# Kernel tuning notes

Hardware: AMD Instinct MI355X
Metric: run time of the kernel (lower is better)

The kernel has to match this reference:

```python
import jax, jax.numpy as jnp
import numpy as np

H = 16          # num_heads
W = 256         # sliding window size
LN_EPS = 1e-6
ROPE_BASE = 10000.0


def layer_norm(x, g, b):
    m = jnp.mean(x, axis=-1, keepdims=True)
    v = jnp.mean((x - m) ** 2, axis=-1, keepdims=True)
    return (x - m) * jax.lax.rsqrt(v + LN_EPS) * g + b


def rope(x):
    # x: [B, S, H, hd]; rotate-half RoPE
    S, hd = x.shape[1], x.shape[-1]
    inv_freq = 1.0 / (ROPE_BASE ** (jnp.arange(0, hd, 2, dtype=jnp.float32) / hd))
    ang = jnp.arange(S, dtype=jnp.float32)[:, None] * inv_freq[None, :]  # [S, hd/2]
    cos = jnp.concatenate([jnp.cos(ang), jnp.cos(ang)], axis=-1)[None, :, None, :]
    sin = jnp.concatenate([jnp.sin(ang), jnp.sin(ang)], axis=-1)[None, :, None, :]
    x1, x2 = jnp.split(x, 2, axis=-1)
    rot = jnp.concatenate([-x2, x1], axis=-1)
    return x * cos + rot * sin


def setup_inputs() -> dict:
    key = jax.random.key(0)
    ks = jax.random.split(key, 12)
    B, S, D, I = 2, 2048, 1024, 4096
    s = 0.02
    return {
        "hidden_states": jax.random.normal(ks[0], (B, S, D), jnp.float32),
        "wq": jax.random.normal(ks[1], (D, D), jnp.float32) * s,
        "wk": jax.random.normal(ks[2], (D, D), jnp.float32) * s,
        "wv": jax.random.normal(ks[3], (D, D), jnp.float32) * s,
        "wo": jax.random.normal(ks[4], (D, D), jnp.float32) * s,
        "w1": jax.random.normal(ks[5], (D, I), jnp.float32) * s,
        "w2": jax.random.normal(ks[6], (I, D), jnp.float32) * s,
        "w3": jax.random.normal(ks[7], (D, I), jnp.float32) * s,
        "ln1_g": jnp.ones((D,), jnp.float32),
        "ln1_b": jnp.zeros((D,), jnp.float32),
        "ln2_g": jnp.ones((D,), jnp.float32),
        "ln2_b": jnp.zeros((D,), jnp.float32),
    }


def reference(hidden_states, wq, wk, wv, wo, w1, w2, w3, ln1_g, ln1_b, ln2_g, ln2_b):
    B, S, D = hidden_states.shape
    hd = D // H

    # --- attention sub-block ---
    residual = hidden_states
    x = layer_norm(hidden_states, ln1_g, ln1_b)
    q = (x @ wq).reshape(B, S, H, hd)
    k = (x @ wk).reshape(B, S, H, hd)
    v = (x @ wv).reshape(B, S, H, hd)
    q, k = rope(q), rope(k)

    scores = jnp.einsum("bqhd,bkhd->bhqk", q, k) / jnp.sqrt(jnp.float32(hd))
    idx = jnp.arange(S)
    rel = idx[:, None] - idx[None, :]          # i - j
    mask = (rel >= 0) & (rel < W)              # causal sliding window
    scores = jnp.where(mask[None, None], scores, jnp.float32(-1e9))
    attn = jax.nn.softmax(scores, axis=-1)
    ctx = jnp.einsum("bhqk,bkhd->bqhd", attn, v).reshape(B, S, D)
    hidden_states = residual + ctx @ wo

    # --- SwiGLU MLP sub-block ---
    residual = hidden_states
    x = layer_norm(hidden_states, ln2_g, ln2_b)
    mlp = (jax.nn.silu(x @ w1) * (x @ w3)) @ w2
    return residual + mlp
```

## Files before the change

### kernel.cpp

```cpp
#include <hip/hip_runtime.h>
#include <hip/hip_bf16.h>

typedef __bf16 bf16_t;
typedef __bf16 bf16x4 __attribute__((ext_vector_type(4)));
typedef __bf16 bf16x8 __attribute__((ext_vector_type(8)));
typedef float f32x4 __attribute__((ext_vector_type(4)));

#define LN_EPS 1e-6f

__device__ __forceinline__ void gl2lds16(const void* g, void* l) {
    __builtin_amdgcn_global_load_lds(
        (const __attribute__((address_space(1))) void*)g,
        (__attribute__((address_space(3))) void*)l, 16, 0, 0);
}

__global__ void transpose_cvt_kernel(const float* __restrict__ in, bf16_t* __restrict__ out,
                                     int R, int C) {
    __shared__ float tile[32][33];
    int tx = threadIdx.x & 31;
    int ty = threadIdx.x >> 5;
    int r0 = blockIdx.y * 32;
    int c0 = blockIdx.x * 32;
#pragma unroll
    for (int i = 0; i < 4; i++) {
        int r = ty + i * 8;
        tile[r][tx] = in[(size_t)(r0 + r) * C + (c0 + tx)];
    }
    __syncthreads();
#pragma unroll
    for (int i = 0; i < 4; i++) {
        int r = ty + i * 8;
        out[(size_t)(c0 + r) * R + (r0 + tx)] = (bf16_t)tile[tx][r];
    }
}

__global__ void ln_kernel(const float* __restrict__ x, const float* __restrict__ g,
                          const float* __restrict__ bb, bf16_t* __restrict__ out, int D) {
    int row = blockIdx.x;
    int t = threadIdx.x;
    const float4* xr = reinterpret_cast<const float4*>(x + (size_t)row * D);
    float4 v = xr[t];
    float s = v.x + v.y + v.z + v.w;
    __shared__ float sbuf[4];
    __shared__ float sbuf2[4];
    int wave = t >> 6, lane = t & 63;
#pragma unroll
    for (int o = 32; o > 0; o >>= 1) s += __shfl_xor(s, o);
    if (lane == 0) sbuf[wave] = s;
    __syncthreads();
    float mean = (sbuf[0] + sbuf[1] + sbuf[2] + sbuf[3]) / (float)D;
    float d0 = v.x - mean, d1 = v.y - mean, d2 = v.z - mean, d3 = v.w - mean;
    float sq = d0 * d0 + d1 * d1 + d2 * d2 + d3 * d3;
#pragma unroll
    for (int o = 32; o > 0; o >>= 1) sq += __shfl_xor(sq, o);
    if (lane == 0) sbuf2[wave] = sq;
    __syncthreads();
    float var = (sbuf2[0] + sbuf2[1] + sbuf2[2] + sbuf2[3]) / (float)D;
    float inv = rsqrtf(var + LN_EPS);
    float4 gv = reinterpret_cast<const float4*>(g)[t];
    float4 bv = reinterpret_cast<const float4*>(bb)[t];
    bf16_t* o0 = out + (size_t)row * D + t * 4;
    o0[0] = (bf16_t)(d0 * inv * gv.x + bv.x);
    o0[1] = (bf16_t)(d1 * inv * gv.y + bv.y);
    o0[2] = (bf16_t)(d2 * inv * gv.z + bv.z);
    o0[3] = (bf16_t)(d3 * inv * gv.w + bv.w);
}

#define G4_BK 64

template <int EPI>
__launch_bounds__(256, 2) __global__
void gemm4_kernel(const bf16_t* __restrict__ A, const bf16_t* __restrict__ Bt,
                  float* __restrict__ Cf, const float* __restrict__ aux,
                  const bf16_t* __restrict__ auxb, bf16_t* __restrict__ Cb,
                  int M, int N, int K, int lda, int ldb) {
    __shared__ __align__(16) bf16_t As[128 * G4_BK];
    __shared__ __align__(16) bf16_t Bs[128 * G4_BK];
    const int t = threadIdx.x;
    const int wave = t >> 6, lane = t & 63;
    const int lr = lane & 15, quad = lane >> 4;
    const int wm = (wave >> 1) * 64, wn = (wave & 1) * 64;

    const int gx = gridDim.x, gy = gridDim.y;
    const int nwg = gx * gy;
    const int lin = blockIdx.y * gx + blockIdx.x;
    const int qch = nwg >> 3;
    const int sw = (lin & 7) * qch + (lin >> 3);
    const int m0 = (sw / gy) * 128;
    const int n0 = (sw % gy) * 128;
    const int koff = blockIdx.z * K;

    const int srow = t >> 3;
    const int sslot = (t & 7) ^ (srow & 7);
    const bf16_t* agp = A + (size_t)(m0 + srow) * lda + koff + sslot * 8;
    const bf16_t* bgp = Bt + (size_t)(n0 + srow) * ldb + koff + sslot * 8;
    bf16_t* asl = As + t * 8;
    bf16_t* bsl = Bs + t * 8;

    int aoff[4][2], boff[4][2];
#pragma unroll
    for (int f = 0; f < 4; f++)
#pragma unroll
        for (int s = 0; s < 2; s++) {
            int ra = wm + f * 16 + lr;
            int rb = wn + f * 16 + lr;
            aoff[f][s] = ra * G4_BK + (((s * 4 + quad) ^ (ra & 7)) << 3);
            boff[f][s] = rb * G4_BK + (((s * 4 + quad) ^ (rb & 7)) << 3);
        }

    f32x4 acc[4][4];
#pragma unroll
    for (int mi = 0; mi < 4; mi++)
#pragma unroll
        for (int ni = 0; ni < 4; ni++) acc[mi][ni] = 0.f;

    for (int k0 = 0; k0 < K; k0 += G4_BK) {
#pragma unroll
        for (int i = 0; i < 4; i++)
            gl2lds16(agp + k0 + (size_t)(32 * i) * lda, asl + i * 2048);
#pragma unroll
        for (int i = 0; i < 4; i++)
            gl2lds16(bgp + k0 + (size_t)(32 * i) * ldb, bsl + i * 2048);
        __syncthreads();
#pragma unroll
        for (int s = 0; s < 2; s++) {
            bf16x8 af[4], bfv[4];
#pragma unroll
            for (int mi = 0; mi < 4; mi++)
                af[mi] = *reinterpret_cast<const bf16x8*>(&As[aoff[mi][s]]);
#pragma unroll
            for (int ni = 0; ni < 4; ni++)
                bfv[ni] = *reinterpret_cast<const bf16x8*>(&Bs[boff[ni][s]]);
#pragma unroll
            for (int mi = 0; mi < 4; mi++)
#pragma unroll
                for (int ni = 0; ni < 4; ni++)
                    acc[mi][ni] = __builtin_amdgcn_mfma_f32_16x16x32_bf16(af[mi], bfv[ni],
                                                                          acc[mi][ni], 0, 0, 0);
        }
        __syncthreads();
    }

    if constexpr (EPI == 3) {
        const float kfreq = -0.41524101186f;
        const int cw = n0 + wn;
        bool do_rope = (cw < 2048);
#pragma unroll
        for (int mi = 0; mi < 4; mi++) {
#pragma unroll
            for (int j = 0; j < 4; j++) {
                int gm = m0 + wm + mi * 16 + quad * 4 + j;
                if (do_rope) {
                    float pos = (float)(gm & 2047);
#pragma unroll
                    for (int p = 0; p < 2; p++) {
                        float x1 = acc[mi][p][j];
                        float x2 = acc[mi][p + 2][j];
                        int d = p * 16 + lr;
                        float freq = exp2f((float)d * kfreq);
                        float ang = pos * freq;
                        float sn, cs;
                        __sincosf(ang, &sn, &cs);
                        size_t idx = (size_t)gm * N + cw + d;
                        Cb[idx] = (bf16_t)(x1 * cs - x2 * sn);
                        Cb[idx + 32] = (bf16_t)(x2 * cs + x1 * sn);
                    }
                } else {
#pragma unroll
                    for (int ni = 0; ni < 4; ni++) {
                        size_t idx = (size_t)gm * N + cw + ni * 16 + lr;
                        Cb[idx] = (bf16_t)acc[mi][ni][j];
                    }
                }
            }
        }
    } else {
        size_t outoff = (EPI == 5) ? (size_t)blockIdx.z * M * N : 0;
#pragma unroll
        for (int mi = 0; mi < 4; mi++)
#pragma unroll
            for (int ni = 0; ni < 4; ni++)
#pragma unroll
                for (int j = 0; j < 4; j++) {
                    int gm = m0 + wm + mi * 16 + quad * 4 + j;
                    int gn = n0 + wn + ni * 16 + lr;
                    size_t idx = (size_t)gm * N + gn;
                    float val = acc[mi][ni][j];
                    if constexpr (EPI == 1) {
                        Cf[idx] = val + aux[idx];
                    } else if constexpr (EPI == 2) {
                        float a = (float)auxb[idx];
                        float sl = a / (1.0f + __expf(-a));
                        Cb[idx] = (bf16_t)(sl * val);
                    } else if constexpr (EPI == 4) {
                        Cb[idx] = (bf16_t)val;
                    } else if constexpr (EPI == 5) {
                        Cb[outoff + idx] = (bf16_t)val;
                    }
                }
    }
}

__global__ void reduce2_kernel(const bf16_t* __restrict__ p, const float* __restrict__ hid,
                               float* __restrict__ out, int n4) {
    int i = blockIdx.x * 256 + threadIdx.x;
    if (i >= n4) return;
    size_t i4 = (size_t)i * 4;
    float4 h = *reinterpret_cast<const float4*>(hid + i4);
    const size_t stride = (size_t)4096 * 1024;
#pragma unroll
    for (int c = 0; c < 2; c++) {
        bf16x4 a = *reinterpret_cast<const bf16x4*>(p + c * stride + i4);
        h.x += (float)a[0];
        h.y += (float)a[1];
        h.z += (float)a[2];
        h.w += (float)a[3];
    }
    *reinterpret_cast<float4*>(out + i4) = h;
}

__global__ void transpose_v_kernel(const bf16_t* __restrict__ v, bf16_t* __restrict__ vt,
                                   int S, int stride) {
    __shared__ bf16_t tile[64][66];
    int t = threadIdx.x;
    int s0 = blockIdx.x * 64;
    int h = blockIdx.y, b = blockIdx.z;
#pragma unroll
    for (int i = 0; i < 2; i++) {
        int c = t + i * 256;
        int ss = c >> 3, d8 = (c & 7) * 8;
        bf16x8 val = *reinterpret_cast<const bf16x8*>(
            &v[(size_t)(b * S + s0 + ss) * stride + h * 64 + d8]);
#pragma unroll
        for (int jj = 0; jj < 8; jj++) tile[ss][d8 + jj] = val[jj];
    }
    __syncthreads();
#pragma unroll
    for (int i = 0; i < 2; i++) {
        int c = t + i * 256;
        int d = c >> 3, s8 = (c & 7) * 8;
        bf16x8 o;
#pragma unroll
        for (int jj = 0; jj < 8; jj++) o[jj] = tile[s8 + jj][d];
        *reinterpret_cast<bf16x8*>(&vt[(((size_t)(b * 16 + h)) * 64 + d) * S + s0 + s8]) = o;
    }
}

#define PSTR 40
#define QKVS 3072
__global__ __launch_bounds__(256, 2) void attn_kernel(const bf16_t* __restrict__ qkv,
                                                      const bf16_t* __restrict__ vt,
                                                      bf16_t* __restrict__ ctx, int S) {
    __shared__ __align__(16) bf16_t Pbuf[4][16 * PSTR];
    int t = threadIdx.x;
    int wave = t >> 6, lane = t & 63;
    int col = lane & 15, quad = lane >> 4;
    int h = blockIdx.y, b = blockIdx.z;
    int q0 = blockIdx.x * 64 + wave * 16;

    const bf16_t* qrow = qkv + (size_t)(b * S + q0 + col) * QKVS + h * 64;
    bf16x8 aq0 = *reinterpret_cast<const bf16x8*>(qrow + quad * 8);
    bf16x8 aq1 = *reinterpret_cast<const bf16x8*>(qrow + 32 + quad * 8);

    int jbase = q0 - 256;
    f32x4 sc[18];
#pragma unroll
    for (int kt = 0; kt < 18; kt++) {
        int j = jbase + kt * 16 + col;
        int jc = j < 0 ? 0 : (j > S - 1 ? S - 1 : j);
        const bf16_t* krow = qkv + (size_t)(b * S + jc) * QKVS + 1024 + h * 64;
        bf16x8 bk0 = *reinterpret_cast<const bf16x8*>(krow + quad * 8);
        bf16x8 bk1 = *reinterpret_cast<const bf16x8*>(krow + 32 + quad * 8);
        f32x4 c0 = {0.f, 0.f, 0.f, 0.f};
        c0 = __builtin_amdgcn_mfma_f32_16x16x32_bf16(aq0, bk0, c0, 0, 0, 0);
        c0 = __builtin_amdgcn_mfma_f32_16x16x32_bf16(aq1, bk1, c0, 0, 0, 0);
        sc[kt] = c0;
    }
#pragma unroll
    for (int kt = 0; kt < 18; kt++) {
#pragma unroll
        for (int jj = 0; jj < 4; jj++) {
            int qq = quad * 4 + jj;
            int j = jbase + kt * 16 + col;
            int rel = (q0 + qq) - j;
            bool ok = (j >= 0) && (rel >= 0) && (rel < 256);
            sc[kt][jj] = ok ? sc[kt][jj] * 0.125f : -1e30f;
        }
    }
    float sminv[4];
#pragma unroll
    for (int jj = 0; jj < 4; jj++) {
        float m = -1e30f;
#pragma unroll
        for (int kt = 0; kt < 18; kt++) m = fmaxf(m, sc[kt][jj]);
#pragma unroll
        for (int o = 1; o < 16; o <<= 1) m = fmaxf(m, __shfl_xor(m, o));
        float s = 0.f;
#pragma unroll
        for (int kt = 0; kt < 18; kt++) {
            float p = __expf(sc[kt][jj] - m);
            sc[kt][jj] = p;
            s += p;
        }
#pragma unroll
        for (int o = 1; o < 16; o <<= 1) s += __shfl_xor(s, o);
        sminv[jj] = 1.0f / s;
    }
    f32x4 o[4];
#pragma unroll
    for (int n = 0; n < 4; n++) o[n] = 0.f;
    bf16_t* myP = Pbuf[wave];
    const bf16_t* vplane = vt + ((size_t)(b * 16 + h)) * 64 * S;
#pragma unroll
    for (int c = 0; c < 9; c++) {
#pragma unroll
        for (int half = 0; half < 2; half++) {
            int kt = 2 * c + half;
#pragma unroll
            for (int jj = 0; jj < 4; jj++) {
                int qq = quad * 4 + jj;
                myP[qq * PSTR + half * 16 + col] = (bf16_t)(sc[kt][jj] * sminv[jj]);
            }
        }
        bf16x8 ap = *reinterpret_cast<const bf16x8*>(myP + col * PSTR + quad * 8);
        int key0 = jbase + c * 32 + quad * 8;
        int kc = key0 < 0 ? 0 : (key0 > S - 8 ? S - 8 : key0);
#pragma unroll
        for (int n = 0; n < 4; n++) {
            bf16x8 bv = *reinterpret_cast<const bf16x8*>(vplane + ((size_t)(n * 16 + col)) * S + kc);
            o[n] = __builtin_amdgcn_mfma_f32_16x16x32_bf16(ap, bv, o[n], 0, 0, 0);
        }
    }
#pragma unroll
    for (int n = 0; n < 4; n++)
#pragma unroll
        for (int jj = 0; jj < 4; jj++) {
            int qq = quad * 4 + jj;
            ctx[((size_t)(b * S + q0 + qq) * 16 + h) * 64 + n * 16 + col] = (bf16_t)o[n][jj];
        }
}

extern "C" void kernel_launch(void* const* d_in, const int* in_sizes, int n_in,
                              void* d_out, int out_size, void* d_ws, size_t ws_size,
                              hipStream_t stream) {
    const float* hs   = (const float*)d_in[0];
    const float* wq   = (const float*)d_in[1];
    const float* wk   = (const float*)d_in[2];
    const float* wv   = (const float*)d_in[3];
    const float* wo   = (const float*)d_in[4];
    const float* w1   = (const float*)d_in[5];
    const float* w2   = (const float*)d_in[6];
    const float* w3   = (const float*)d_in[7];
    const float* ln1g = (const float*)d_in[8];
    const float* ln1b = (const float*)d_in[9];
    const float* ln2g = (const float*)d_in[10];
    const float* ln2b = (const float*)d_in[11];
    float* out = (float*)d_out;

    const int B = 2, S = 2048, D = 1024, I = 4096;
    const int BS = B * S;

    char* ws = (char*)d_ws;
    const size_t MB = 1024 * 1024;
    bf16_t* wq_t = (bf16_t*)(ws + 0 * MB);
    bf16_t* wk_t = (bf16_t*)(ws + 2 * MB);
    bf16_t* wv_t = (bf16_t*)(ws + 4 * MB);
    bf16_t* wo_t = (bf16_t*)(ws + 6 * MB);
    bf16_t* w1_t = (bf16_t*)(ws + 8 * MB);
    bf16_t* w3_t = (bf16_t*)(ws + 16 * MB);
    bf16_t* w2_t = (bf16_t*)(ws + 24 * MB);
    bf16_t* x_b  = (bf16_t*)(ws + 32 * MB);
    float*  hid  = (float*)(ws + 40 * MB);
    bf16_t* x2_b = (bf16_t*)(ws + 56 * MB);
    bf16_t* qkvb = (bf16_t*)(ws + 64 * MB);
    bf16_t* vt   = (bf16_t*)(ws + 88 * MB);
    bf16_t* ctxb = (bf16_t*)(ws + 96 * MB);
    bf16_t* h1b  = (bf16_t*)(ws + 64 * MB);
    bf16_t* hbuf = (bf16_t*)(ws + 96 * MB);
    bf16_t* pker = (bf16_t*)(ws + 64 * MB);

    dim3 tb(256);
    transpose_cvt_kernel<<<dim3(D / 32, D / 32), tb, 0, stream>>>(wq, wq_t, D, D);
    transpose_cvt_kernel<<<dim3(D / 32, D / 32), tb, 0, stream>>>(wk, wk_t, D, D);
    transpose_cvt_kernel<<<dim3(D / 32, D / 32), tb, 0, stream>>>(wv, wv_t, D, D);
    transpose_cvt_kernel<<<dim3(D / 32, D / 32), tb, 0, stream>>>(wo, wo_t, D, D);
    transpose_cvt_kernel<<<dim3(I / 32, D / 32), tb, 0, stream>>>(w1, w1_t, D, I);
    transpose_cvt_kernel<<<dim3(I / 32, D / 32), tb, 0, stream>>>(w3, w3_t, D, I);
    transpose_cvt_kernel<<<dim3(D / 32, I / 32), tb, 0, stream>>>(w2, w2_t, I, D);

    ln_kernel<<<BS, tb, 0, stream>>>(hs, ln1g, ln1b, x_b, D);

    gemm4_kernel<3><<<dim3(BS / 128, 3072 / 128), tb, 0, stream>>>(
        x_b, wq_t, nullptr, nullptr, nullptr, qkvb, BS, 3072, D, D, D);

    transpose_v_kernel<<<dim3(S / 64, 16, B), tb, 0, stream>>>(qkvb + 2048, vt, S, QKVS);

    attn_kernel<<<dim3(S / 64, 16, B), tb, 0, stream>>>(qkvb, vt, ctxb, S);

    gemm4_kernel<1><<<dim3(BS / 128, D / 128), tb, 0, stream>>>(
        ctxb, wo_t, hid, hs, nullptr, nullptr, BS, D, D, D, D);

    ln_kernel<<<BS, tb, 0, stream>>>(hid, ln2g, ln2b, x2_b, D);

    gemm4_kernel<4><<<dim3(BS / 128, I / 128), tb, 0, stream>>>(
        x2_b, w1_t, nullptr, nullptr, nullptr, h1b, BS, I, D, D, D);
    gemm4_kernel<2><<<dim3(BS / 128, I / 128), tb, 0, stream>>>(
        x2_b, w3_t, nullptr, nullptr, h1b, hbuf, BS, I, D, D, D);

    gemm4_kernel<5><<<dim3(BS / 128, D / 128, 2), tb, 0, stream>>>(
        hbuf, w2_t, nullptr, nullptr, nullptr, pker, BS, D, 2048, I, I);
    reduce2_kernel<<<dim3(BS * D / 4 / 256), tb, 0, stream>>>(pker, hid, out, BS * D / 4);
}
```

Measured before the change: 388.8 us.

## Add 256x256-tile 8-wave GEMM with staged LDS pipelining for QKV and MLP

Introduces a new GEMM kernel that uses 256x256 output tiles, 512 threads, and a double-buffered 128KB LDS. The A and B tiles are staged in halves with direct global-to-LDS loads, overlapped with MFMA phases, and ordered with explicit waitcnt/barriers, setprio and a grouped workgroup swizzle. The QKV+RoPE, w1, w3 and w2 GEMMs switch to this kernel, and the w2 split-K goes from 2 to 4 partitions with a matching reduce. Larger tiles cut global traffic per flop, but there are fewer workgroups (e.g. 192 for QKV) on a large-CU GPU, plus more register pressure and a bigger split-K reduction.

```diff
diff --git a/kernel.cpp b/kernel.cpp
--- a/kernel.cpp
+++ b/kernel.cpp
@@ -12,6 +12,12 @@
     __builtin_amdgcn_global_load_lds(
         (const __attribute__((address_space(1))) void*)g,
         (__attribute__((address_space(3))) void*)l, 16, 0, 0);
+}
+
+__device__ __forceinline__ void block_sync() {
+    __asm__ __volatile__("" ::: "memory");
+    __builtin_amdgcn_s_barrier();
+    __asm__ __volatile__("" ::: "memory");
 }
 
 __global__ void transpose_cvt_kernel(const float* __restrict__ in, bf16_t* __restrict__ out,
@@ -141,67 +147,240 @@
         __syncthreads();
     }
 
+#pragma unroll
+    for (int mi = 0; mi < 4; mi++)
+#pragma unroll
+        for (int ni = 0; ni < 4; ni++)
+#pragma unroll
+            for (int j = 0; j < 4; j++) {
+                int gm = m0 + wm + mi * 16 + quad * 4 + j;
+                int gn = n0 + wn + ni * 16 + lr;
+                size_t idx = (size_t)gm * N + gn;
+                float val = acc[mi][ni][j];
+                if constexpr (EPI == 1) {
+                    Cf[idx] = val + aux[idx];
+                }
+            }
+}
+
+
+__device__ __forceinline__ void stage_half(const bf16_t* g, int ld, bf16_t* l,
+                                           int wave, int lane) {
+#pragma unroll
+    for (int i = 0; i < 2; i++) {
+        int lidx = (wave * 2 + i) * 64 + lane;
+        int row = lidx >> 3;
+        int ss = (lidx & 7) ^ (row & 7);
+        gl2lds16(g + (size_t)row * ld + ss * 8, l + (wave * 2 + i) * 512);
+    }
+}
+
+template <int QM, int QN>
+__device__ __forceinline__ void quad_mfma(f32x4 (&acc)[2][2][4][2], const bf16x8 (&af)[4][2],
+                                          const bf16x8 (&bf)[2][2]) {
+#pragma unroll
+    for (int fr = 0; fr < 4; fr++)
+#pragma unroll
+        for (int fc = 0; fc < 2; fc++)
+#pragma unroll
+            for (int ks = 0; ks < 2; ks++)
+                acc[QM][QN][fr][fc] = __builtin_amdgcn_mfma_f32_16x16x32_bf16(
+                    af[fr][ks], bf[fc][ks], acc[QM][QN][fr][fc], 0, 0, 0);
+}
+
+template <int EPI>
+__launch_bounds__(512, 2) __global__
+void gemm5_kernel(const bf16_t* __restrict__ A, const bf16_t* __restrict__ Bt,
+                  const bf16_t* __restrict__ auxb, bf16_t* __restrict__ Cb,
+                  int M, int N, int K, int lda, int ldb) {
+    extern __shared__ __align__(16) bf16_t smem[];
+    bf16_t* smA = smem;
+    bf16_t* smB = smem + 32768;
+    const int t = threadIdx.x;
+    const int wave = t >> 6, lane = t & 63;
+    const int lr = lane & 15, quad = lane >> 4;
+    const int rowgrp = wave >> 2;
+    const int colgrp = wave & 3;
+    const int cg1 = colgrp & 1, cg2 = colgrp >> 1;
+
+    const int gx = gridDim.x, gy = gridDim.y;
+    const int nwg = gx * gy;
+    const int lin = blockIdx.y * gx + blockIdx.x;
+    const int qch = nwg >> 3;
+    const int sw = (lin & 7) * qch + (lin >> 3);
+    const int m0 = (sw / gy) * 256;
+    const int n0 = (sw % gy) * 256;
+    const int koff = blockIdx.z * K;
+
+    const bf16_t* Ag = A + (size_t)m0 * lda + koff;
+    const bf16_t* Bg = Bt + (size_t)n0 * ldb + koff;
+
+    int aoff[4][2], boff[2][2];
+#pragma unroll
+    for (int fr = 0; fr < 4; fr++)
+#pragma unroll
+        for (int ks = 0; ks < 2; ks++) {
+            int ra = rowgrp * 64 + fr * 16 + lr;
+            aoff[fr][ks] = ra * 64 + (((ks * 4 + quad) ^ (ra & 7)) << 3);
+        }
+#pragma unroll
+    for (int fc = 0; fc < 2; fc++)
+#pragma unroll
+        for (int ks = 0; ks < 2; ks++) {
+            int rb = cg1 * 64 + cg2 * 16 + fc * 32 + lr;
+            boff[fc][ks] = rb * 64 + (((ks * 4 + quad) ^ (rb & 7)) << 3);
+        }
+
+    f32x4 acc[2][2][4][2];
+#pragma unroll
+    for (int qm = 0; qm < 2; qm++)
+#pragma unroll
+        for (int qn = 0; qn < 2; qn++)
+#pragma unroll
+            for (int fr = 0; fr < 4; fr++)
+#pragma unroll
+                for (int fc = 0; fc < 2; fc++) acc[qm][qn][fr][fc] = 0.f;
+
+    stage_half(Ag, lda, smA, wave, lane);
+    stage_half(Bg, ldb, smB, wave, lane);
+    stage_half(Bg + (size_t)128 * ldb, ldb, smB + 8192, wave, lane);
+    stage_half(Ag + (size_t)128 * lda, lda, smA + 8192, wave, lane);
+    __asm__ __volatile__("s_waitcnt vmcnt(4)" ::: "memory");
+    block_sync();
+
+    const int NT = K >> 6;
+    bf16x8 af[4][2], bf0[2][2], bf1[2][2];
+
+    for (int tt = 0; tt < NT; ++tt) {
+        const int cur = tt & 1, nxt = cur ^ 1;
+        const bf16_t* A0b = smA + cur * 16384;
+        const bf16_t* A1b = A0b + 8192;
+        const bf16_t* B0b = smB + cur * 16384;
+        const bf16_t* B1b = B0b + 8192;
+        bf16_t* sA0n = smA + nxt * 16384;
+        bf16_t* sB0n = smB + nxt * 16384;
+        const bool pf = (tt + 1 < NT);
+        const size_t kn = (size_t)(tt + 1) << 6;
+
+#pragma unroll
+        for (int fr = 0; fr < 4; fr++)
+#pragma unroll
+            for (int ks = 0; ks < 2; ks++)
+                af[fr][ks] = *reinterpret_cast<const bf16x8*>(A0b + aoff[fr][ks]);
+#pragma unroll
+        for (int fc = 0; fc < 2; fc++)
+#pragma unroll
+            for (int ks = 0; ks < 2; ks++)
+                bf0[fc][ks] = *reinterpret_cast<const bf16x8*>(B0b + boff[fc][ks]);
+        if (pf) {
+            stage_half(Ag + kn, lda, sA0n, wave, lane);
+            stage_half(Bg + kn, ldb, sB0n, wave, lane);
+        }
+        block_sync();
+        __asm__ __volatile__("s_waitcnt lgkmcnt(0)" ::: "memory");
+        __builtin_amdgcn_sched_barrier(0);
+        __builtin_amdgcn_s_setprio(1);
+        quad_mfma<0, 0>(acc, af, bf0);
+        __builtin_amdgcn_s_setprio(0);
+        __asm__ __volatile__("s_waitcnt vmcnt(6)" ::: "memory");
+        block_sync();
+
+#pragma unroll
+        for (int fc = 0; fc < 2; fc++)
+#pragma unroll
+            for (int ks = 0; ks < 2; ks++)
+                bf1[fc][ks] = *reinterpret_cast<const bf16x8*>(B1b + boff[fc][ks]);
+        if (pf) stage_half(Bg + (size_t)128 * ldb + kn, ldb, sB0n + 8192, wave, lane);
+        block_sync();
+        __asm__ __volatile__("s_waitcnt lgkmcnt(0)" ::: "memory");
+        __builtin_amdgcn_sched_barrier(0);
+        __builtin_amdgcn_s_setprio(1);
+        quad_mfma<0, 1>(acc, af, bf1);
+        __builtin_amdgcn_s_setprio(0);
+        __asm__ __volatile__("s_waitcnt vmcnt(6)" ::: "memory");
+        block_sync();
+
+#pragma unroll
+        for (int fr = 0; fr < 4; fr++)
+#pragma unroll
+            for (int ks = 0; ks < 2; ks++)
+                af[fr][ks] = *reinterpret_cast<const bf16x8*>(A1b + aoff[fr][ks]);
+        if (pf) stage_half(Ag + (size_t)128 * lda + kn, lda, sA0n + 8192, wave, lane);
+        block_sync();
+        __asm__ __volatile__("s_waitcnt lgkmcnt(0)" ::: "memory");
+        __builtin_amdgcn_sched_barrier(0);
+        __builtin_amdgcn_s_setprio(1);
+        quad_mfma<1, 1>(acc, af, bf1);
+        quad_mfma<1, 0>(acc, af, bf0);
+        __builtin_amdgcn_s_setprio(0);
+        __asm__ __volatile__("s_waitcnt vmcnt(4)" ::: "memory");
+        block_sync();
+    }
+
     if constexpr (EPI == 3) {
         const float kfreq = -0.41524101186f;
-        const int cw = n0 + wn;
-        bool do_rope = (cw < 2048);
-#pragma unroll
-        for (int mi = 0; mi < 4; mi++) {
-#pragma unroll
-            for (int j = 0; j < 4; j++) {
-                int gm = m0 + wm + mi * 16 + quad * 4 + j;
-                if (do_rope) {
-                    float pos = (float)(gm & 2047);
-#pragma unroll
-                    for (int p = 0; p < 2; p++) {
-                        float x1 = acc[mi][p][j];
-                        float x2 = acc[mi][p + 2][j];
-                        int d = p * 16 + lr;
-                        float freq = exp2f((float)d * kfreq);
-                        float ang = pos * freq;
-                        float sn, cs;
-                        __sincosf(ang, &sn, &cs);
-                        size_t idx = (size_t)gm * N + cw + d;
-                        Cb[idx] = (bf16_t)(x1 * cs - x2 * sn);
-                        Cb[idx + 32] = (bf16_t)(x2 * cs + x1 * sn);
+        bool do_rope = (n0 + 128 < 2048 + 1);
+        const int d = cg2 * 16 + lr;
+        const float freq = exp2f((float)d * kfreq);
+#pragma unroll
+        for (int qm = 0; qm < 2; qm++)
+#pragma unroll
+            for (int qn = 0; qn < 2; qn++) {
+                const int gnb = n0 + qn * 128 + cg1 * 64;
+#pragma unroll
+                for (int fr = 0; fr < 4; fr++)
+#pragma unroll
+                    for (int j = 0; j < 4; j++) {
+                        int gm = m0 + qm * 128 + rowgrp * 64 + fr * 16 + quad * 4 + j;
+                        if (do_rope) {
+                            float pos = (float)(gm & 2047);
+                            float ang = pos * freq;
+                            float sn, cs;
+                            __sincosf(ang, &sn, &cs);
+                            float x1 = acc[qm][qn][fr][0][j];
+                            float x2 = acc[qm][qn][fr][1][j];
+                            size_t idx = (size_t)gm * N + gnb + d;
+                            Cb[idx] = (bf16_t)(x1 * cs - x2 * sn);
+                            Cb[idx + 32] = (bf16_t)(x2 * cs + x1 * sn);
+                        } else {
+#pragma unroll
+                            for (int fc = 0; fc < 2; fc++) {
+                                size_t idx = (size_t)gm * N + gnb + cg2 * 16 + fc * 32 + lr;
+                                Cb[idx] = (bf16_t)acc[qm][qn][fr][fc][j];
+                            }
+                        }
                     }
-                } else {
-#pragma unroll
-                    for (int ni = 0; ni < 4; ni++) {
-                        size_t idx = (size_t)gm * N + cw + ni * 16 + lr;
-                        Cb[idx] = (bf16_t)acc[mi][ni][j];
-                    }
-                }
             }
-        }
     } else {
         size_t outoff = (EPI == 5) ? (size_t)blockIdx.z * M * N : 0;
 #pragma unroll
-        for (int mi = 0; mi < 4; mi++)
-#pragma unroll
-            for (int ni = 0; ni < 4; ni++)
-#pragma unroll
-                for (int j = 0; j < 4; j++) {
-                    int gm = m0 + wm + mi * 16 + quad * 4 + j;
-                    int gn = n0 + wn + ni * 16 + lr;
-                    size_t idx = (size_t)gm * N + gn;
-                    float val = acc[mi][ni][j];
-                    if constexpr (EPI == 1) {
-                        Cf[idx] = val + aux[idx];
-                    } else if constexpr (EPI == 2) {
-                        float a = (float)auxb[idx];
-                        float sl = a / (1.0f + __expf(-a));
-                        Cb[idx] = (bf16_t)(sl * val);
-                    } else if constexpr (EPI == 4) {
-                        Cb[idx] = (bf16_t)val;
-                    } else if constexpr (EPI == 5) {
-                        Cb[outoff + idx] = (bf16_t)val;
-                    }
-                }
-    }
-}
-
-__global__ void reduce2_kernel(const bf16_t* __restrict__ p, const float* __restrict__ hid,
+        for (int qm = 0; qm < 2; qm++)
+#pragma unroll
+            for (int qn = 0; qn < 2; qn++)
+#pragma unroll
+                for (int fr = 0; fr < 4; fr++)
+#pragma unroll
+                    for (int fc = 0; fc < 2; fc++)
+#pragma unroll
+                        for (int j = 0; j < 4; j++) {
+                            int gm = m0 + qm * 128 + rowgrp * 64 + fr * 16 + quad * 4 + j;
+                            int gn = n0 + qn * 128 + cg1 * 64 + cg2 * 16 + fc * 32 + lr;
+                            size_t idx = (size_t)gm * N + gn;
+                            float val = acc[qm][qn][fr][fc][j];
+                            if constexpr (EPI == 2) {
+                                float a = (float)auxb[idx];
+                                float sl = a / (1.0f + __expf(-a));
+                                Cb[idx] = (bf16_t)(sl * val);
+                            } else if constexpr (EPI == 4) {
+                                Cb[idx] = (bf16_t)val;
+                            } else if constexpr (EPI == 5) {
+                                Cb[outoff + idx] = (bf16_t)val;
+                            }
+                        }
+    }
+}
+
+__global__ void reduce4_kernel(const bf16_t* __restrict__ p, const float* __restrict__ hid,
                                float* __restrict__ out, int n4) {
     int i = blockIdx.x * 256 + threadIdx.x;
     if (i >= n4) return;
@@ -209,7 +388,7 @@
     float4 h = *reinterpret_cast<const float4*>(hid + i4);
     const size_t stride = (size_t)4096 * 1024;
 #pragma unroll
-    for (int c = 0; c < 2; c++) {
+    for (int c = 0; c < 4; c++) {
         bf16x4 a = *reinterpret_cast<const bf16x4*>(p + c * stride + i4);
         h.x += (float)a[0];
         h.y += (float)a[1];
@@ -379,7 +558,17 @@
     bf16_t* hbuf = (bf16_t*)(ws + 96 * MB);
     bf16_t* pker = (bf16_t*)(ws + 64 * MB);
 
+    hipFuncSetAttribute(reinterpret_cast<const void*>(&gemm5_kernel<2>),
+                        hipFuncAttributeMaxDynamicSharedMemorySize, 131072);
+    hipFuncSetAttribute(reinterpret_cast<const void*>(&gemm5_kernel<3>),
+                        hipFuncAttributeMaxDynamicSharedMemorySize, 131072);
+    hipFuncSetAttribute(reinterpret_cast<const void*>(&gemm5_kernel<4>),
+                        hipFuncAttributeMaxDynamicSharedMemorySize, 131072);
+    hipFuncSetAttribute(reinterpret_cast<const void*>(&gemm5_kernel<5>),
+                        hipFuncAttributeMaxDynamicSharedMemorySize, 131072);
+
     dim3 tb(256);
+    dim3 tb5(512);
     transpose_cvt_kernel<<<dim3(D / 32, D / 32), tb, 0, stream>>>(wq, wq_t, D, D);
     transpose_cvt_kernel<<<dim3(D / 32, D / 32), tb, 0, stream>>>(wk, wk_t, D, D);
     transpose_cvt_kernel<<<dim3(D / 32, D / 32), tb, 0, stream>>>(wv, wv_t, D, D);
@@ -390,8 +579,8 @@
 
     ln_kernel<<<BS, tb, 0, stream>>>(hs, ln1g, ln1b, x_b, D);
 
-    gemm4_kernel<3><<<dim3(BS / 128, 3072 / 128), tb, 0, stream>>>(
-        x_b, wq_t, nullptr, nullptr, nullptr, qkvb, BS, 3072, D, D, D);
+    gemm5_kernel<3><<<dim3(BS / 256, 3072 / 256), tb5, 131072, stream>>>(
+        x_b, wq_t, nullptr, qkvb, BS, 3072, D, D, D);
 
     transpose_v_kernel<<<dim3(S / 64, 16, B), tb, 0, stream>>>(qkvb + 2048, vt, S, QKVS);
 
@@ -402,12 +591,12 @@
 
     ln_kernel<<<BS, tb, 0, stream>>>(hid, ln2g, ln2b, x2_b, D);
 
-    gemm4_kernel<4><<<dim3(BS / 128, I / 128), tb, 0, stream>>>(
-        x2_b, w1_t, nullptr, nullptr, nullptr, h1b, BS, I, D, D, D);
-    gemm4_kernel<2><<<dim3(BS / 128, I / 128), tb, 0, stream>>>(
-        x2_b, w3_t, nullptr, nullptr, h1b, hbuf, BS, I, D, D, D);
-
-    gemm4_kernel<5><<<dim3(BS / 128, D / 128, 2), tb, 0, stream>>>(
-        hbuf, w2_t, nullptr, nullptr, nullptr, pker, BS, D, 2048, I, I);
-    reduce2_kernel<<<dim3(BS * D / 4 / 256), tb, 0, stream>>>(pker, hid, out, BS * D / 4);
-}
+    gemm5_kernel<4><<<dim3(BS / 256, I / 256), tb5, 131072, stream>>>(
+        x2_b, w1_t, nullptr, h1b, BS, I, D, D, D);
+    gemm5_kernel<2><<<dim3(BS / 256, I / 256), tb5, 131072, stream>>>(
+        x2_b, w3_t, h1b, hbuf, BS, I, D, D, D);
+
+    gemm5_kernel<5><<<dim3(BS / 256, D / 256, 4), tb5, 131072, stream>>>(
+        hbuf, w2_t, nullptr, pker, BS, D, 1024, I, I);
+    reduce4_kernel<<<dim3(BS * D / 4 / 256), tb, 0, stream>>>(pker, hid, out, BS * D / 4);
+}
```

Result: faster. 379.6 us (-2.4%).
